# Kernel tuning notes

Hardware: AMD Instinct MI355X
Metric: run time of the kernel (lower is better)

Reference implementation:

```python
import jax, jax.numpy as jnp
import numpy as np

D_MODEL = 1024
NUM_HEADS = 16
HEAD_DIM = D_MODEL // NUM_HEADS
SEQ_LEN = 2048
THETA = 10000.0


def setup_inputs() -> dict:
    key = jax.random.key(0)
    ks = jax.random.split(key, 9)
    s = 1.0 / np.sqrt(D_MODEL)
    inp = {
        "x": jax.random.normal(ks[0], (2, SEQ_LEN, D_MODEL), dtype=jnp.float32),
        "Wq": jax.random.uniform(ks[1], (D_MODEL, D_MODEL), jnp.float32, -s, s),
        "bq": jax.random.uniform(ks[2], (D_MODEL,), jnp.float32, -s, s),
        "Wk": jax.random.uniform(ks[3], (D_MODEL, D_MODEL), jnp.float32, -s, s),
        "bk": jax.random.uniform(ks[4], (D_MODEL,), jnp.float32, -s, s),
        "Wv": jax.random.uniform(ks[5], (D_MODEL, D_MODEL), jnp.float32, -s, s),
        "bv": jax.random.uniform(ks[6], (D_MODEL,), jnp.float32, -s, s),
        "Wo": jax.random.uniform(ks[7], (D_MODEL, D_MODEL), jnp.float32, -s, s),
        "bo": jax.random.uniform(ks[8], (D_MODEL,), jnp.float32, -s, s),
    }
    return inp


def _rope_cos_sin(seq_len, dim, theta):
    inv_freq = 1.0 / theta ** (jnp.arange(0, dim, 2, dtype=jnp.float32) / dim)  # [dim/2]
    t = jnp.arange(seq_len, dtype=jnp.float32)
    freqs = jnp.outer(t, inv_freq)  # [S, dim/2]
    return jnp.cos(freqs), jnp.sin(freqs)


def _apply_rope(x, cos, sin):
    # x: [B, H, S, head_dim]; interleaved complex pairs (even, odd)
    x2 = x.reshape(*x.shape[:-1], -1, 2)  # [B,H,S,hd/2,2]
    xe, xo = x2[..., 0], x2[..., 1]
    c = cos[None, None, :, :]
    s = sin[None, None, :, :]
    oe = xe * c - xo * s
    oo = xe * s + xo * c
    return jnp.stack([oe, oo], axis=-1).reshape(x.shape)


def reference(x, Wq, bq, Wk, bk, Wv, bv, Wo, bo):
    B, S, D = x.shape
    H, hd = NUM_HEADS, HEAD_DIM
    q = x @ Wq.T + bq
    k = x @ Wk.T + bk
    v = x @ Wv.T + bv
    # [B, H, S, hd]
    q = q.reshape(B, S, H, hd).transpose(0, 2, 1, 3)
    k = k.reshape(B, S, H, hd).transpose(0, 2, 1, 3)
    v = v.reshape(B, S, H, hd).transpose(0, 2, 1, 3)
    cos, sin = _rope_cos_sin(S, hd, THETA)
    q = _apply_rope(q, cos, sin)
    k = _apply_rope(k, cos, sin)
    scores = jnp.einsum("bhqd,bhkd->bhqk", q, k) / jnp.sqrt(jnp.float32(hd))
    causal = jnp.triu(jnp.ones((S, S), dtype=bool), k=1)
    scores = jnp.where(causal[None, None, :, :], -jnp.inf, scores)
    attn = jax.nn.softmax(scores, axis=-1)
    out = jnp.einsum("bhqk,bhkd->bhqd", attn, v)
    out = out.transpose(0, 2, 1, 3).reshape(B, S, D)
    return out @ Wo.T + bo
```

## Files before the change

### kernel.cpp

```cpp
#include <hip/hip_runtime.h>
#include <hip/hip_bf16.h>

#define S_LEN 2048
#define DM 1024
#define NH 16
#define HD 64
#define M_ROWS 4096
#define LOG2E 1.4426950408889634f
#define MASKVAL -1.0e4f

typedef __attribute__((ext_vector_type(8))) short short8;
typedef __attribute__((ext_vector_type(4))) float f32x4;
typedef __attribute__((ext_vector_type(16))) float f32x16;

__device__ inline ushort f2b(float f) {
  union { float f; unsigned u; } v; v.f = f;
  unsigned r = v.u + 0x7fffu + ((v.u >> 16) & 1u);
  return (ushort)(r >> 16);
}

__device__ inline float b2f(ushort u) {
  union { unsigned u; float f; } v; v.u = ((unsigned)u) << 16; return v.f;
}

__device__ inline unsigned pk_bf16(float a, float b) {
  __hip_bfloat162 h = __float22bfloat162_rn(make_float2(a, b));
  union { __hip_bfloat162 h; unsigned u; } v; v.h = h;
  return v.u;
}

__device__ inline float fexp2(float x) { return __builtin_amdgcn_exp2f(x); }

__device__ inline void gl_lds16(const void* g, void* l) {
  __builtin_amdgcn_global_load_lds(
      (const __attribute__((address_space(1))) void*)g,
      (__attribute__((address_space(3))) void*)l, 16, 0, 0);
}

__global__ __launch_bounds__(256) void cast_all_kernel(
    const float* __restrict__ x, const float* __restrict__ Wq, const float* __restrict__ Wk,
    const float* __restrict__ Wv, const float* __restrict__ Wo,
    ushort* __restrict__ xb, ushort* __restrict__ Wqb, ushort* __restrict__ Wkb,
    ushort* __restrict__ Wvb, ushort* __restrict__ Wob) {
  int i = blockIdx.x * 256 + threadIdx.x;
  int r = i >> 18, off = i & 0x3FFFF;
  const float4* s;
  uint2* d;
  switch (r) {
    case 0: case 1: case 2: case 3: s = (const float4*)x + i;  d = (uint2*)xb + i;  break;
    case 4: s = (const float4*)Wq + off; d = (uint2*)Wqb + off; break;
    case 5: s = (const float4*)Wk + off; d = (uint2*)Wkb + off; break;
    case 6: s = (const float4*)Wv + off; d = (uint2*)Wvb + off; break;
    default: s = (const float4*)Wo + off; d = (uint2*)Wob + off; break;
  }
  float4 v = *s;
  uint2 o;
  o.x = pk_bf16(v.x, v.y);
  o.y = pk_bf16(v.z, v.w);
  *d = o;
}

__global__ __launch_bounds__(256) void rope_table_kernel(float* __restrict__ C, float* __restrict__ Sn) {
  int idx = blockIdx.x * blockDim.x + threadIdx.x;
  int s = idx >> 5, i = idx & 31;
  float inv = exp2f(-(float)i * (13.287712379549449f / 32.0f));
  float a = (float)s * inv;
  C[idx] = cosf(a);
  Sn[idx] = sinf(a);
}

__global__ __launch_bounds__(256) void gemm_qkv_kernel(const ushort* __restrict__ xb,
    const ushort* __restrict__ Wqb, const ushort* __restrict__ Wkb, const ushort* __restrict__ Wvb,
    const float* __restrict__ bq, const float* __restrict__ bk, const float* __restrict__ bv,
    const float* __restrict__ ropeC, const float* __restrict__ ropeS,
    ushort* __restrict__ qb, ushort* __restrict__ kb, ushort* __restrict__ vT) {
  __shared__ ushort lds[128 * 136];
  ushort* As = lds;
  ushort* Bs = lds + 8192;
  const int z = blockIdx.z;
  const ushort* W = (z == 0) ? Wqb : ((z == 1) ? Wkb : Wvb);
  const float* bias = (z == 0) ? bq : ((z == 1) ? bk : bv);
  const int m0 = blockIdx.x * 128, n0 = blockIdx.y * 128;
  const int t = threadIdx.x, lane = t & 63, wave = t >> 6;
  const int wr = (wave >> 1) * 64, wc = (wave & 1) * 64;
  const int lr = lane & 15, lg = lane >> 4;

  int rows_[4], gs_[4], slots_[4];
#pragma unroll
  for (int j = 0; j < 4; j++) {
    const int slot = wave * 256 + j * 64 + lane;
    slots_[j] = slot;
    rows_[j] = slot >> 3;
    gs_[j] = (slot & 7) ^ (rows_[j] & 7);
  }

  f32x4 acc[4][4];
#pragma unroll
  for (int a = 0; a < 4; a++)
#pragma unroll
    for (int b = 0; b < 4; b++) acc[a][b] = (f32x4){0.f, 0.f, 0.f, 0.f};

  for (int k0 = 0; k0 < DM; k0 += 64) {
    __syncthreads();
#pragma unroll
    for (int j = 0; j < 4; j++)
      gl_lds16(&xb[(size_t)(m0 + rows_[j]) * DM + k0 + gs_[j] * 8], &As[slots_[j] * 8]);
#pragma unroll
    for (int j = 0; j < 4; j++)
      gl_lds16(&W[(size_t)(n0 + rows_[j]) * DM + k0 + gs_[j] * 8], &Bs[slots_[j] * 8]);
    __syncthreads();
#pragma unroll
    for (int s32 = 0; s32 < 2; s32++) {
      short8 af[4], bf[4];
#pragma unroll
      for (int mt = 0; mt < 4; mt++) {
        const int row = wr + mt * 16 + lr;
        af[mt] = *(const short8*)&As[(row * 8 + ((s32 * 4 + lg) ^ (row & 7))) * 8];
      }
#pragma unroll
      for (int nt = 0; nt < 4; nt++) {
        const int row = wc + nt * 16 + lr;
        bf[nt] = *(const short8*)&Bs[(row * 8 + ((s32 * 4 + lg) ^ (row & 7))) * 8];
      }
#pragma unroll
      for (int mt = 0; mt < 4; mt++)
#pragma unroll
        for (int nt = 0; nt < 4; nt++)
          acc[mt][nt] = __builtin_amdgcn_mfma_f32_16x16x32_bf16(af[mt], bf[nt], acc[mt][nt], 0, 0, 0);
    }
  }

  __syncthreads();
#pragma unroll
  for (int mt = 0; mt < 4; mt++) {
#pragma unroll
    for (int nt = 0; nt < 4; nt++) {
      const int nloc = wc + nt * 16 + lr;
      const float bn = bias[n0 + nloc];
#pragma unroll
      for (int r = 0; r < 4; r++) {
        const int mloc = wr + mt * 16 + lg * 4 + r;
        const ushort v = f2b(acc[mt][nt][r] + bn);
        if (z < 2) lds[mloc * 136 + nloc] = v;
        else       lds[nloc * 136 + mloc] = v;
      }
    }
  }
  __syncthreads();

  const int b = m0 >> 11;
  if (z < 2) {
    ushort* dst = (z == 0) ? qb : kb;
    const float qscale = (z == 0) ? 0.125f : 1.0f;
#pragma unroll
    for (int c = 0; c < 8; c++) {
      const int sloc = c * 16 + (t >> 4);
      const int nloc = (t & 15) * 8;
      short8 val = *(const short8*)&lds[sloc * 136 + nloc];
      const int s = (m0 + sloc) & (S_LEN - 1);
      const int h = (n0 + nloc) >> 6;
      const int d0 = nloc & 63;
      const float4 cv = *(const float4*)&ropeC[s * 32 + d0 / 2];
      const float4 sv = *(const float4*)&ropeS[s * 32 + d0 / 2];
      uint4 o;
      {
        float e = b2f((ushort)val[0]), od = b2f((ushort)val[1]);
        o.x = pk_bf16((e * cv.x - od * sv.x) * qscale, (e * sv.x + od * cv.x) * qscale);
      }
      {
        float e = b2f((ushort)val[2]), od = b2f((ushort)val[3]);
        o.y = pk_bf16((e * cv.y - od * sv.y) * qscale, (e * sv.y + od * cv.y) * qscale);
      }
      {
        float e = b2f((ushort)val[4]), od = b2f((ushort)val[5]);
        o.z = pk_bf16((e * cv.z - od * sv.z) * qscale, (e * sv.z + od * cv.z) * qscale);
      }
      {
        float e = b2f((ushort)val[6]), od = b2f((ushort)val[7]);
        o.w = pk_bf16((e * cv.w - od * sv.w) * qscale, (e * sv.w + od * cv.w) * qscale);
      }
      *(uint4*)&dst[(((size_t)b * NH + h) * S_LEN + s) * HD + d0] = o;
    }
  } else {
    const int sbase = m0 & (S_LEN - 1);
#pragma unroll
    for (int c = 0; c < 8; c++) {
      const int nloc = c * 16 + (t >> 4);
      const int s0 = (t & 15) * 8;
      short8 val = *(const short8*)&lds[nloc * 136 + s0];
      const int h = (n0 + nloc) >> 6;
      const int d = nloc & 63;
      *(short8*)&vT[(((size_t)b * NH + h) * HD + d) * S_LEN + sbase + s0] = val;
    }
  }
}

__global__ __launch_bounds__(256) void flash_kernel(const ushort* __restrict__ qb,
                                                    const ushort* __restrict__ kb,
                                                    const ushort* __restrict__ vT,
                                                    ushort* __restrict__ Oh,
                                                    float2* __restrict__ ml) {
  __shared__ ushort Ks[2][4096];
  __shared__ ushort VTs[2][4096];
  const int t = threadIdx.x, lane = t & 63, wave = t >> 6;
  const int q31 = lane & 31, h = lane >> 5;
  const int y = blockIdx.y;
  const int bh = y >> 1, half = y & 1;
  const int qt = (y & 16) ? (int)blockIdx.x : (15 - (int)blockIdx.x);
  const int q0 = qt * 128;
  const ushort* kbh = kb + (size_t)bh * S_LEN * HD;
  const ushort* vbh = vT + (size_t)bh * HD * S_LEN;

  const int qrow = q0 + wave * 32 + q31;
  const ushort* qptr = qb + ((size_t)bh * S_LEN + qrow) * HD + h * 8;
  short8 qf[4];
#pragma unroll
  for (int s = 0; s < 4; s++) qf[s] = *(const short8*)(qptr + s * 16);

  const int slot0 = wave * 128 + lane, slot1 = slot0 + 64;
  const int row0 = slot0 >> 3, g0 = (slot0 & 7) ^ (row0 & 7);
  const int row1 = slot1 >> 3, g1 = (slot1 & 7) ^ (row1 & 7);
  const int lo0 = wave * 128 * 8, lo1 = lo0 + 64 * 8;

  {
    const int k00 = half * 64;
    gl_lds16(kbh + (size_t)(k00 + row0) * HD + g0 * 8, &Ks[0][lo0]);
    gl_lds16(kbh + (size_t)(k00 + row1) * HD + g1 * 8, &Ks[0][lo1]);
    gl_lds16(vbh + (size_t)row0 * S_LEN + k00 + g0 * 8, &VTs[0][lo0]);
    gl_lds16(vbh + (size_t)row1 * S_LEN + k00 + g1 * 8, &VTs[0][lo1]);
  }
  __syncthreads();

  f32x16 O[2];
#pragma unroll
  for (int st = 0; st < 2; st++)
#pragma unroll
    for (int r = 0; r < 16; r++) O[st][r] = 0.f;
  float m_i = MASKVAL, l_i = 0.f;
  int cur = 0;

  for (int idx = 0; idx <= qt; idx++) {
    const int kt = half + 2 * idx;
    if (idx < qt) {
      const int k0n = (kt + 2) * 64;
      gl_lds16(kbh + (size_t)(k0n + row0) * HD + g0 * 8, &Ks[cur ^ 1][lo0]);
      gl_lds16(kbh + (size_t)(k0n + row1) * HD + g1 * 8, &Ks[cur ^ 1][lo1]);
      gl_lds16(vbh + (size_t)row0 * S_LEN + k0n + g0 * 8, &VTs[cur ^ 1][lo0]);
      gl_lds16(vbh + (size_t)row1 * S_LEN + k0n + g1 * 8, &VTs[cur ^ 1][lo1]);
    }
    const ushort* Kb = Ks[cur];
    const ushort* Vb = VTs[cur];

    f32x16 sc[2];
#pragma unroll
    for (int st = 0; st < 2; st++)
#pragma unroll
      for (int r = 0; r < 16; r++) sc[st][r] = 0.f;
#pragma unroll
    for (int s = 0; s < 4; s++) {
#pragma unroll
      for (int st = 0; st < 2; st++) {
        const int row = st * 32 + q31;
        const short8 kf = *(const short8*)&Kb[(row * 8 + ((2 * s + h) ^ (row & 7))) * 8];
        sc[st] = __builtin_amdgcn_mfma_f32_32x32x16_bf16(kf, qf[s], sc[st], 0, 0, 0);
      }
    }
    if (kt * 64 + 63 > q0 + wave * 32) {
#pragma unroll
      for (int st = 0; st < 2; st++)
#pragma unroll
        for (int r = 0; r < 16; r++) {
          const int kcol = kt * 64 + st * 32 + (r & 3) + 8 * (r >> 2) + 4 * h;
          if (kcol > qrow) sc[st][r] = MASKVAL;
        }
    }
    float mx = sc[0][0];
#pragma unroll
    for (int st = 0; st < 2; st++)
#pragma unroll
      for (int r = 0; r < 16; r++) mx = fmaxf(mx, sc[st][r]);
    mx = fmaxf(mx, __shfl_xor(mx, 32));
    const float mnew = fmaxf(m_i, mx);
    const float alpha = fexp2((m_i - mnew) * LOG2E);
    const float nmw = -mnew * LOG2E;
    float su = 0.f;
#pragma unroll
    for (int st = 0; st < 2; st++)
#pragma unroll
      for (int r = 0; r < 16; r++) {
        const float p = fexp2(fmaf(sc[st][r], LOG2E, nmw));
        sc[st][r] = p;
        su += p;
      }
    su += __shfl_xor(su, 32);
    l_i = l_i * alpha + su;
    m_i = mnew;
#pragma unroll
    for (int st = 0; st < 2; st++)
#pragma unroll
      for (int r = 0; r < 16; r++) O[st][r] *= alpha;

    unsigned pp[8][2];
#pragma unroll
    for (int st = 0; st < 2; st++)
#pragma unroll
      for (int rg = 0; rg < 4; rg++) {
        pp[st * 4 + rg][0] = pk_bf16(sc[st][4 * rg + 0], sc[st][4 * rg + 1]);
        pp[st * 4 + rg][1] = pk_bf16(sc[st][4 * rg + 2], sc[st][4 * rg + 3]);
      }
#pragma unroll
    for (int s = 0; s < 4; s++) {
      const unsigned sA0 = pp[2 * s][0], sA1 = pp[2 * s][1];
      const unsigned sB0 = pp[2 * s + 1][0], sB1 = pp[2 * s + 1][1];
      const unsigned send0 = h ? sA0 : sB0;
      const unsigned send1 = h ? sA1 : sB1;
      const unsigned recv0 = (unsigned)__shfl_xor((int)send0, 32);
      const unsigned recv1 = (unsigned)__shfl_xor((int)send1, 32);
      union { unsigned u[4]; short8 v; } pf;
      pf.u[0] = h ? recv0 : sA0;
      pf.u[1] = h ? recv1 : sA1;
      pf.u[2] = h ? sB0 : recv0;
      pf.u[3] = h ? sB1 : recv1;
#pragma unroll
      for (int st = 0; st < 2; st++) {
        const int row = st * 32 + q31;
        const short8 vf = *(const short8*)&Vb[(row * 8 + ((2 * s + h) ^ (row & 7))) * 8];
        O[st] = __builtin_amdgcn_mfma_f32_32x32x16_bf16(vf, pf.v, O[st], 0, 0, 0);
      }
    }
    __syncthreads();
    cur ^= 1;
  }

  ushort* obase = Oh + (((size_t)half * 32 + bh) * S_LEN + qrow) * HD;
#pragma unroll
  for (int st = 0; st < 2; st++)
#pragma unroll
    for (int rg = 0; rg < 4; rg++) {
      const int d0 = st * 32 + 8 * rg + 4 * h;
      uint2 w;
      w.x = pk_bf16(O[st][4 * rg + 0], O[st][4 * rg + 1]);
      w.y = pk_bf16(O[st][4 * rg + 2], O[st][4 * rg + 3]);
      *(uint2*)&obase[d0] = w;
    }
  if (h == 0) ml[((size_t)half * 32 + bh) * S_LEN + qrow] = make_float2(m_i, l_i);
}

__global__ __launch_bounds__(256) void combine_kernel(const ushort* __restrict__ Oh,
                                                      const float2* __restrict__ ml,
                                                      ushort* __restrict__ attn) {
  const int tid = blockIdx.x * 256 + threadIdx.x;
  const int d8 = tid & 7;
  const int q = (tid >> 3) & (S_LEN - 1);
  const int bh = tid >> 14;
  const float2 ml0 = ml[(size_t)bh * S_LEN + q];
  const float2 ml1 = ml[((size_t)32 + bh) * S_LEN + q];
  const float m = fmaxf(ml0.x, ml1.x);
  const float w0 = fexp2((ml0.x - m) * LOG2E);
  const float w1 = fexp2((ml1.x - m) * LOG2E);
  const float inv = 1.f / (ml0.y * w0 + ml1.y * w1);
  const uint4 a = *(const uint4*)&Oh[((size_t)bh * S_LEN + q) * HD + d8 * 8];
  const uint4 bb = *(const uint4*)&Oh[(((size_t)32 + bh) * S_LEN + q) * HD + d8 * 8];
  const unsigned au[4] = {a.x, a.y, a.z, a.w};
  const unsigned bu[4] = {bb.x, bb.y, bb.z, bb.w};
  uint4 o;
  unsigned* op = (unsigned*)&o;
#pragma unroll
  for (int j = 0; j < 4; j++) {
    const float a0 = b2f((ushort)(au[j] & 0xffff)), a1 = b2f((ushort)(au[j] >> 16));
    const float b0 = b2f((ushort)(bu[j] & 0xffff)), b1 = b2f((ushort)(bu[j] >> 16));
    op[j] = pk_bf16((a0 * w0 + b0 * w1) * inv, (a1 * w0 + b1 * w1) * inv);
  }
  const int b = bh >> 4, hh = bh & 15;
  *(uint4*)&attn[((size_t)b * S_LEN + q) * DM + hh * HD + d8 * 8] = o;
}

__global__ __launch_bounds__(256) void gemm_out_kernel(const ushort* __restrict__ attn,
                                                       const ushort* __restrict__ Wob,
                                                       const float* __restrict__ bo,
                                                       float* __restrict__ out) {
  __shared__ ushort As[4096];
  __shared__ ushort Bs[2048];
  const int m0 = blockIdx.x * 128, n0 = blockIdx.y * 64;
  const int t = threadIdx.x, lane = t & 63, wave = t >> 6;
  const int wm = (wave >> 1) * 64, wn = (wave & 1) * 32;
  const int lr = lane & 15, lg = lane >> 4;
  const int slotA0 = wave * 128 + lane, slotA1 = slotA0 + 64;
  const int rowA0 = slotA0 >> 2, gA0 = (slotA0 & 3) ^ (rowA0 & 3);
  const int rowA1 = slotA1 >> 2, gA1 = (slotA1 & 3) ^ (rowA1 & 3);
  const int slotB = wave * 64 + lane;
  const int rowB = slotB >> 2, gB = (slotB & 3) ^ (rowB & 3);

  f32x4 acc[4][2];
#pragma unroll
  for (int a = 0; a < 4; a++)
#pragma unroll
    for (int b = 0; b < 2; b++) acc[a][b] = (f32x4){0.f, 0.f, 0.f, 0.f};

  for (int k0 = 0; k0 < DM; k0 += 32) {
    __syncthreads();
    gl_lds16(&attn[(size_t)(m0 + rowA0) * DM + k0 + gA0 * 8], &As[slotA0 * 8]);
    gl_lds16(&attn[(size_t)(m0 + rowA1) * DM + k0 + gA1 * 8], &As[slotA1 * 8]);
    gl_lds16(&Wob[(size_t)(n0 + rowB) * DM + k0 + gB * 8], &Bs[slotB * 8]);
    __syncthreads();
    short8 af[4], bf[2];
#pragma unroll
    for (int mt = 0; mt < 4; mt++) {
      const int row = wm + mt * 16 + lr;
      af[mt] = *(const short8*)&As[(row * 4 + (lg ^ (row & 3))) * 8];
    }
#pragma unroll
    for (int nt = 0; nt < 2; nt++) {
      const int row = wn + nt * 16 + lr;
      bf[nt] = *(const short8*)&Bs[(row * 4 + (lg ^ (row & 3))) * 8];
    }
#pragma unroll
    for (int mt = 0; mt < 4; mt++)
#pragma unroll
      for (int nt = 0; nt < 2; nt++)
        acc[mt][nt] = __builtin_amdgcn_mfma_f32_16x16x32_bf16(af[mt], bf[nt], acc[mt][nt], 0, 0, 0);
  }

#pragma unroll
  for (int mt = 0; mt < 4; mt++) {
#pragma unroll
    for (int nt = 0; nt < 2; nt++) {
      const int n = n0 + wn + nt * 16 + lr;
      const float bn = bo[n];
#pragma unroll
      for (int r = 0; r < 4; r++) {
        const int m = m0 + wm + mt * 16 + lg * 4 + r;
        out[(size_t)m * DM + n] = acc[mt][nt][r] + bn;
      }
    }
  }
}

extern "C" void kernel_launch(void* const* d_in, const int* in_sizes, int n_in,
                              void* d_out, int out_size, void* d_ws, size_t ws_size,
                              hipStream_t stream) {
  const float* x  = (const float*)d_in[0];
  const float* Wq = (const float*)d_in[1];
  const float* bq = (const float*)d_in[2];
  const float* Wk = (const float*)d_in[3];
  const float* bk = (const float*)d_in[4];
  const float* Wv = (const float*)d_in[5];
  const float* bv = (const float*)d_in[6];
  const float* Wo = (const float*)d_in[7];
  const float* bo = (const float*)d_in[8];
  float* out = (float*)d_out;

  char* ws = (char*)d_ws;
  size_t off = 0;
  auto alloc = [&](size_t bytes) { char* p = ws + off; off += (bytes + 255) & ~255ull; return p; };
  ushort* xb   = (ushort*)alloc((size_t)M_ROWS * DM * 2);
  ushort* Wqb  = (ushort*)alloc((size_t)DM * DM * 2);
  ushort* Wkb  = (ushort*)alloc((size_t)DM * DM * 2);
  ushort* Wvb  = (ushort*)alloc((size_t)DM * DM * 2);
  ushort* Wob  = (ushort*)alloc((size_t)DM * DM * 2);
  ushort* qb   = (ushort*)alloc((size_t)M_ROWS * DM * 2);
  ushort* kb   = (ushort*)alloc((size_t)M_ROWS * DM * 2);
  ushort* vTb  = (ushort*)alloc((size_t)M_ROWS * DM * 2);
  ushort* attn = (ushort*)alloc((size_t)M_ROWS * DM * 2);
  ushort* Ohb  = (ushort*)alloc((size_t)2 * 32 * S_LEN * HD * 2);
  float2* mlb  = (float2*)alloc((size_t)2 * 32 * S_LEN * 8);
  float* ropeC = (float*)alloc((size_t)S_LEN * 32 * 4);
  float* ropeS = (float*)alloc((size_t)S_LEN * 32 * 4);
  (void)ws_size; (void)in_sizes; (void)n_in; (void)out_size;

  cast_all_kernel<<<8192, 256, 0, stream>>>(x, Wq, Wk, Wv, Wo, xb, Wqb, Wkb, Wvb, Wob);
  rope_table_kernel<<<(S_LEN * 32) / 256, 256, 0, stream>>>(ropeC, ropeS);
  gemm_qkv_kernel<<<dim3(M_ROWS / 128, DM / 128, 3), 256, 0, stream>>>(
      xb, Wqb, Wkb, Wvb, bq, bk, bv, ropeC, ropeS, qb, kb, vTb);
  flash_kernel<<<dim3(16, 64), 256, 0, stream>>>(qb, kb, vTb, Ohb, mlb);
  combine_kernel<<<2048, 256, 0, stream>>>(Ohb, mlb, attn);
  gemm_out_kernel<<<dim3(M_ROWS / 128, DM / 64), 256, 0, stream>>>(attn, Wob, bo, out);
}
```

Baseline: 212.1 us.

## Split causal attention into balanced KV chunks and drop online-softmax max tracking

```diff
diff --git a/kernel.cpp b/kernel.cpp
--- a/kernel.cpp
+++ b/kernel.cpp
@@ -8,6 +8,7 @@
 #define M_ROWS 4096
 #define LOG2E 1.4426950408889634f
 #define MASKVAL -1.0e4f
+#define QSCALE 0.18033688011112042f
 
 typedef __attribute__((ext_vector_type(8))) short short8;
 typedef __attribute__((ext_vector_type(4))) float f32x4;
@@ -37,12 +38,23 @@
       (__attribute__((address_space(3))) void*)l, 16, 0, 0);
 }
 
-__global__ __launch_bounds__(256) void cast_all_kernel(
+__global__ __launch_bounds__(256) void cast_rope_kernel(
     const float* __restrict__ x, const float* __restrict__ Wq, const float* __restrict__ Wk,
     const float* __restrict__ Wv, const float* __restrict__ Wo,
     ushort* __restrict__ xb, ushort* __restrict__ Wqb, ushort* __restrict__ Wkb,
-    ushort* __restrict__ Wvb, ushort* __restrict__ Wob) {
-  int i = blockIdx.x * 256 + threadIdx.x;
+    ushort* __restrict__ Wvb, ushort* __restrict__ Wob,
+    float* __restrict__ ropeC, float* __restrict__ ropeS) {
+  const int bid = blockIdx.x;
+  if (bid >= 8192) {
+    int idx = (bid - 8192) * 256 + threadIdx.x;
+    int s = idx >> 5, i = idx & 31;
+    float inv = exp2f(-(float)i * (13.287712379549449f / 32.0f));
+    float a = (float)s * inv;
+    ropeC[idx] = cosf(a);
+    ropeS[idx] = sinf(a);
+    return;
+  }
+  int i = bid * 256 + threadIdx.x;
   int r = i >> 18, off = i & 0x3FFFF;
   const float4* s;
   uint2* d;
@@ -58,15 +70,6 @@
   o.x = pk_bf16(v.x, v.y);
   o.y = pk_bf16(v.z, v.w);
   *d = o;
-}
-
-__global__ __launch_bounds__(256) void rope_table_kernel(float* __restrict__ C, float* __restrict__ Sn) {
-  int idx = blockIdx.x * blockDim.x + threadIdx.x;
-  int s = idx >> 5, i = idx & 31;
-  float inv = exp2f(-(float)i * (13.287712379549449f / 32.0f));
-  float a = (float)s * inv;
-  C[idx] = cosf(a);
-  Sn[idx] = sinf(a);
 }
 
 __global__ __launch_bounds__(256) void gemm_qkv_kernel(const ushort* __restrict__ xb,
@@ -151,7 +154,7 @@
   const int b = m0 >> 11;
   if (z < 2) {
     ushort* dst = (z == 0) ? qb : kb;
-    const float qscale = (z == 0) ? 0.125f : 1.0f;
+    const float qscale = (z == 0) ? QSCALE : 1.0f;
 #pragma unroll
     for (int c = 0; c < 8; c++) {
       const int sloc = c * 16 + (t >> 4);
@@ -199,15 +202,25 @@
                                                     const ushort* __restrict__ kb,
                                                     const ushort* __restrict__ vT,
                                                     ushort* __restrict__ Oh,
-                                                    float2* __restrict__ ml) {
+                                                    float* __restrict__ lsum) {
   __shared__ ushort Ks[2][4096];
   __shared__ ushort VTs[2][4096];
   const int t = threadIdx.x, lane = t & 63, wave = t >> 6;
   const int q31 = lane & 31, h = lane >> 5;
-  const int y = blockIdx.y;
-  const int bh = y >> 1, half = y & 1;
-  const int qt = (y & 16) ? (int)blockIdx.x : (15 - (int)blockIdx.x);
+  const int bh = blockIdx.y;
+  const int cid = blockIdx.x;
+  const int g = (cid >= 24) ? 3 : (cid >= 12) ? 2 : (cid >= 4) ? 1 : 0;
+  const int nc = g + 1;
+  const int o = cid - 4 * ((g * (g + 1)) >> 1);
+  const int qi = o / nc;
+  const int c = o - qi * nc;
+  const int qt = g * 4 + qi;
   const int q0 = qt * 128;
+  const int ntiles = 2 * qt + 2;
+  const int kstart = c * 8;
+  const int kend = min(kstart + 8, ntiles);
+  const int pidx = bh * 40 + cid;
+
   const ushort* kbh = kb + (size_t)bh * S_LEN * HD;
   const ushort* vbh = vT + (size_t)bh * HD * S_LEN;
 
@@ -222,8 +235,17 @@
   const int row1 = slot1 >> 3, g1 = (slot1 & 7) ^ (row1 & 7);
   const int lo0 = wave * 128 * 8, lo1 = lo0 + 64 * 8;
 
+  int foff[4][2];
+#pragma unroll
+  for (int s = 0; s < 4; s++)
+#pragma unroll
+    for (int st = 0; st < 2; st++) {
+      const int row = st * 32 + q31;
+      foff[s][st] = (row * 8 + ((2 * s + h) ^ (row & 7))) * 8;
+    }
+
   {
-    const int k00 = half * 64;
+    const int k00 = kstart * 64;
     gl_lds16(kbh + (size_t)(k00 + row0) * HD + g0 * 8, &Ks[0][lo0]);
     gl_lds16(kbh + (size_t)(k00 + row1) * HD + g1 * 8, &Ks[0][lo1]);
     gl_lds16(vbh + (size_t)row0 * S_LEN + k00 + g0 * 8, &VTs[0][lo0]);
@@ -236,13 +258,12 @@
   for (int st = 0; st < 2; st++)
 #pragma unroll
     for (int r = 0; r < 16; r++) O[st][r] = 0.f;
-  float m_i = MASKVAL, l_i = 0.f;
+  float lacc = 0.f;
   int cur = 0;
 
-  for (int idx = 0; idx <= qt; idx++) {
-    const int kt = half + 2 * idx;
-    if (idx < qt) {
-      const int k0n = (kt + 2) * 64;
+  for (int kt = kstart; kt < kend; kt++) {
+    if (kt + 1 < kend) {
+      const int k0n = (kt + 1) * 64;
       gl_lds16(kbh + (size_t)(k0n + row0) * HD + g0 * 8, &Ks[cur ^ 1][lo0]);
       gl_lds16(kbh + (size_t)(k0n + row1) * HD + g1 * 8, &Ks[cur ^ 1][lo1]);
       gl_lds16(vbh + (size_t)row0 * S_LEN + k0n + g0 * 8, &VTs[cur ^ 1][lo0]);
@@ -260,8 +281,7 @@
     for (int s = 0; s < 4; s++) {
 #pragma unroll
       for (int st = 0; st < 2; st++) {
-        const int row = st * 32 + q31;
-        const short8 kf = *(const short8*)&Kb[(row * 8 + ((2 * s + h) ^ (row & 7))) * 8];
+        const short8 kf = *(const short8*)&Kb[foff[s][st]];
         sc[st] = __builtin_amdgcn_mfma_f32_32x32x16_bf16(kf, qf[s], sc[st], 0, 0, 0);
       }
     }
@@ -274,31 +294,14 @@
           if (kcol > qrow) sc[st][r] = MASKVAL;
         }
     }
-    float mx = sc[0][0];
 #pragma unroll
     for (int st = 0; st < 2; st++)
 #pragma unroll
-      for (int r = 0; r < 16; r++) mx = fmaxf(mx, sc[st][r]);
-    mx = fmaxf(mx, __shfl_xor(mx, 32));
-    const float mnew = fmaxf(m_i, mx);
-    const float alpha = fexp2((m_i - mnew) * LOG2E);
-    const float nmw = -mnew * LOG2E;
-    float su = 0.f;
-#pragma unroll
-    for (int st = 0; st < 2; st++)
-#pragma unroll
       for (int r = 0; r < 16; r++) {
-        const float p = fexp2(fmaf(sc[st][r], LOG2E, nmw));
+        const float p = fexp2(sc[st][r]);
         sc[st][r] = p;
-        su += p;
-      }
-    su += __shfl_xor(su, 32);
-    l_i = l_i * alpha + su;
-    m_i = mnew;
-#pragma unroll
-    for (int st = 0; st < 2; st++)
-#pragma unroll
-      for (int r = 0; r < 16; r++) O[st][r] *= alpha;
+        lacc += p;
+      }
 
     unsigned pp[8][2];
 #pragma unroll
@@ -323,8 +326,7 @@
       pf.u[3] = h ? sB1 : recv1;
 #pragma unroll
       for (int st = 0; st < 2; st++) {
-        const int row = st * 32 + q31;
-        const short8 vf = *(const short8*)&Vb[(row * 8 + ((2 * s + h) ^ (row & 7))) * 8];
+        const short8 vf = *(const short8*)&Vb[foff[s][st]];
         O[st] = __builtin_amdgcn_mfma_f32_32x32x16_bf16(vf, pf.v, O[st], 0, 0, 0);
       }
     }
@@ -332,7 +334,9 @@
     cur ^= 1;
   }
 
-  ushort* obase = Oh + (((size_t)half * 32 + bh) * S_LEN + qrow) * HD;
+  lacc += __shfl_xor(lacc, 32);
+
+  ushort* obase = Oh + ((size_t)pidx * 128 + wave * 32 + q31) * HD;
 #pragma unroll
   for (int st = 0; st < 2; st++)
 #pragma unroll
@@ -343,34 +347,41 @@
       w.y = pk_bf16(O[st][4 * rg + 2], O[st][4 * rg + 3]);
       *(uint2*)&obase[d0] = w;
     }
-  if (h == 0) ml[((size_t)half * 32 + bh) * S_LEN + qrow] = make_float2(m_i, l_i);
+  if (h == 0) lsum[(size_t)pidx * 128 + wave * 32 + q31] = lacc;
 }
 
 __global__ __launch_bounds__(256) void combine_kernel(const ushort* __restrict__ Oh,
-                                                      const float2* __restrict__ ml,
+                                                      const float* __restrict__ lsum,
                                                       ushort* __restrict__ attn) {
   const int tid = blockIdx.x * 256 + threadIdx.x;
   const int d8 = tid & 7;
   const int q = (tid >> 3) & (S_LEN - 1);
   const int bh = tid >> 14;
-  const float2 ml0 = ml[(size_t)bh * S_LEN + q];
-  const float2 ml1 = ml[((size_t)32 + bh) * S_LEN + q];
-  const float m = fmaxf(ml0.x, ml1.x);
-  const float w0 = fexp2((ml0.x - m) * LOG2E);
-  const float w1 = fexp2((ml1.x - m) * LOG2E);
-  const float inv = 1.f / (ml0.y * w0 + ml1.y * w1);
-  const uint4 a = *(const uint4*)&Oh[((size_t)bh * S_LEN + q) * HD + d8 * 8];
-  const uint4 bb = *(const uint4*)&Oh[(((size_t)32 + bh) * S_LEN + q) * HD + d8 * 8];
-  const unsigned au[4] = {a.x, a.y, a.z, a.w};
-  const unsigned bu[4] = {bb.x, bb.y, bb.z, bb.w};
+  const int qt = q >> 7, row = q & 127;
+  const int g = qt >> 2, nc = g + 1;
+  const int base = 4 * ((g * (g + 1)) >> 1) + (qt & 3) * nc;
+  const int p0 = bh * 40 + base;
+
+  float l = 0.f;
+  float acc[8];
+#pragma unroll
+  for (int j = 0; j < 8; j++) acc[j] = 0.f;
+  for (int c = 0; c < nc; c++) {
+    const size_t rowidx = (size_t)(p0 + c) * 128 + row;
+    l += lsum[rowidx];
+    const uint4 a = *(const uint4*)&Oh[rowidx * HD + d8 * 8];
+    const unsigned au[4] = {a.x, a.y, a.z, a.w};
+#pragma unroll
+    for (int j = 0; j < 4; j++) {
+      acc[2 * j] += b2f((ushort)(au[j] & 0xffff));
+      acc[2 * j + 1] += b2f((ushort)(au[j] >> 16));
+    }
+  }
+  const float inv = 1.f / l;
   uint4 o;
   unsigned* op = (unsigned*)&o;
 #pragma unroll
-  for (int j = 0; j < 4; j++) {
-    const float a0 = b2f((ushort)(au[j] & 0xffff)), a1 = b2f((ushort)(au[j] >> 16));
-    const float b0 = b2f((ushort)(bu[j] & 0xffff)), b1 = b2f((ushort)(bu[j] >> 16));
-    op[j] = pk_bf16((a0 * w0 + b0 * w1) * inv, (a1 * w0 + b1 * w1) * inv);
-  }
+  for (int j = 0; j < 4; j++) op[j] = pk_bf16(acc[2 * j] * inv, acc[2 * j + 1] * inv);
   const int b = bh >> 4, hh = bh & 15;
   *(uint4*)&attn[((size_t)b * S_LEN + q) * DM + hh * HD + d8 * 8] = o;
 }
@@ -462,17 +473,17 @@
   ushort* kb   = (ushort*)alloc((size_t)M_ROWS * DM * 2);
   ushort* vTb  = (ushort*)alloc((size_t)M_ROWS * DM * 2);
   ushort* attn = (ushort*)alloc((size_t)M_ROWS * DM * 2);
-  ushort* Ohb  = (ushort*)alloc((size_t)2 * 32 * S_LEN * HD * 2);
-  float2* mlb  = (float2*)alloc((size_t)2 * 32 * S_LEN * 8);
+  ushort* Ohb  = (ushort*)alloc((size_t)1280 * 128 * HD * 2);
+  float* lsb   = (float*)alloc((size_t)1280 * 128 * 4);
   float* ropeC = (float*)alloc((size_t)S_LEN * 32 * 4);
   float* ropeS = (float*)alloc((size_t)S_LEN * 32 * 4);
   (void)ws_size; (void)in_sizes; (void)n_in; (void)out_size;
 
-  cast_all_kernel<<<8192, 256, 0, stream>>>(x, Wq, Wk, Wv, Wo, xb, Wqb, Wkb, Wvb, Wob);
-  rope_table_kernel<<<(S_LEN * 32) / 256, 256, 0, stream>>>(ropeC, ropeS);
+  cast_rope_kernel<<<8448, 256, 0, stream>>>(x, Wq, Wk, Wv, Wo, xb, Wqb, Wkb, Wvb, Wob,
+                                             ropeC, ropeS);
   gemm_qkv_kernel<<<dim3(M_ROWS / 128, DM / 128, 3), 256, 0, stream>>>(
       xb, Wqb, Wkb, Wvb, bq, bk, bv, ropeC, ropeS, qb, kb, vTb);
-  flash_kernel<<<dim3(16, 64), 256, 0, stream>>>(qb, kb, vTb, Ohb, mlb);
-  combine_kernel<<<2048, 256, 0, stream>>>(Ohb, mlb, attn);
+  flash_kernel<<<dim3(40, 32), 256, 0, stream>>>(qb, kb, vTb, Ohb, lsb);
+  combine_kernel<<<2048, 256, 0, stream>>>(Ohb, lsb, attn);
   gemm_out_kernel<<<dim3(M_ROWS / 128, DM / 64), 256, 0, stream>>>(attn, Wob, bo, out);
 }
```

After: 202.3 us. 1.05x faster.
